# Kernel optimization log

Hardware: AMD Instinct MI355X
Metric: run time of the kernel (lower is better)

## Reference

```python
import jax, jax.numpy as jnp
import numpy as np

B = 4             # graphs per batch
POS_RANGE = 240.0 # pos lives in [0, 240)^3
VOXELS = (20.0, 30.0, 50.0, 80.0)
NEG = -1e30


def _basis(u):
    # open B-spline basis, degree 1, kernel_size 2, dim 3 -> 8 weights per edge
    cols = []
    for k in range(8):
        w = (u[:, 0] if k & 4 else 1.0 - u[:, 0])
        w = w * (u[:, 1] if k & 2 else 1.0 - u[:, 1])
        w = w * (u[:, 2] if k & 1 else 1.0 - u[:, 2])
        cols.append(w)
    return jnp.stack(cols, axis=1)  # [E, 8]


def _cartesian(pos, src, dst, emask):
    # T.Cartesian(cat=False, norm=True): rel pos scaled into [0,1]
    rel = pos[src] - pos[dst]
    m = jnp.max(jnp.where(emask[:, None], jnp.abs(rel), 0.0))
    return rel / (2.0 * jnp.maximum(m, 1e-9)) + 0.5


def _spline_conv(x, src, dst, pseudo, emask, W, Wr, b, n_nodes):
    # out_i = mean_{j->i} sum_k B_k(u_ij) x_j W_k + x_i Wr + b
    basis = _basis(pseudo) * emask[:, None].astype(x.dtype)  # [E,8]
    xk = jnp.einsum('ni,kio->nko', x, W)                     # [N,8,O]
    msg = basis[:, 0, None] * xk[src, 0]
    for k in range(1, 8):
        msg = msg + basis[:, k, None] * xk[src, k]           # [E,O]
    agg = jax.ops.segment_sum(msg, dst, num_segments=n_nodes)
    deg = jax.ops.segment_sum(emask.astype(x.dtype), dst, num_segments=n_nodes)
    return agg / jnp.maximum(deg, 1.0)[:, None] + x @ Wr + b


def _voxel_ids(pos, batch, vs):
    G = int(np.ceil(POS_RANGE / vs))
    c = jnp.clip(jnp.floor(pos / vs).astype(jnp.int64), 0, G - 1)
    cell = (c[:, 0] * G + c[:, 1]) * G + c[:, 2]
    return batch * (G ** 3) + cell, G ** 3


def _max_pool(x, pos, batch, valid, src, dst, emask, vs):
    # voxel-grid max pooling: nodes become fixed voxel cells (empty cells masked)
    nid, ncells = _voxel_ids(pos, batch, vs)
    n_new = B * ncells
    xm = jnp.where(valid[:, None], x, NEG)
    x_p = jax.ops.segment_max(xm, nid, num_segments=n_new)
    cnt = jax.ops.segment_sum(valid.astype(x.dtype), nid, num_segments=n_new)
    v_new = cnt > 0
    x_p = jnp.where(v_new[:, None], x_p, 0.0)
    pos_p = jax.ops.segment_sum(pos * valid[:, None].astype(pos.dtype), nid, num_segments=n_new)
    pos_p = pos_p / jnp.maximum(cnt, 1.0)[:, None]
    batch_p = jnp.arange(n_new, dtype=jnp.int64) // ncells
    # coarsen edges: remap to cells, drop self loops, coalesce at fixed size
    s2, d2 = nid[src], nid[dst]
    sent = n_new * n_new
    key = jnp.where(emask & (s2 != d2), s2 * n_new + d2, sent)
    uk = jnp.unique(key, size=key.shape[0], fill_value=sent)
    em = uk != sent
    uk = jnp.where(em, uk, 0)
    return x_p, pos_p, batch_p, v_new, uk // n_new, uk % n_new, em


def setup_inputs():
    key = jax.random.key(0)
    ks = jax.random.split(key, 24)
    NP, DEG = 5000, 8
    N = B * NP
    E = N * DEG
    x = jax.random.normal(ks[0], (N, 1), dtype=jnp.float32)
    pos = jax.random.uniform(ks[1], (N, 3), dtype=jnp.float32) * POS_RANGE
    src = jnp.repeat(jnp.arange(N, dtype=jnp.int64), DEG)
    delta = jax.random.randint(ks[2], (E,), 1, 100, dtype=jnp.int64)
    dst = (src // NP) * NP + (src % NP + delta) % NP   # intra-graph edges
    edge_index = jnp.stack([src, dst])
    batch = jnp.arange(N, dtype=jnp.int64) // NP
    sizes = [1, 64, 128, 256, 512]
    params = {}
    for l in range(4):
        ci, co = sizes[l], sizes[l + 1]
        params[f'W{l+1}'] = jax.random.normal(ks[3 + 3 * l], (8, ci, co), dtype=jnp.float32) / np.sqrt(8.0 * ci)
        params[f'Wr{l+1}'] = jax.random.normal(ks[4 + 3 * l], (ci, co), dtype=jnp.float32) / np.sqrt(float(ci))
        params[f'b{l+1}'] = jnp.zeros((co,), dtype=jnp.float32)
    params['fc1_w'] = jax.random.normal(ks[16], (64 * 512, 1024), dtype=jnp.float32) / np.sqrt(64.0 * 512.0)
    params['fc1_b'] = jnp.zeros((1024,), dtype=jnp.float32)
    params['fc2_w'] = jax.random.normal(ks[17], (1024, 1), dtype=jnp.float32) / np.sqrt(1024.0)
    params['fc2_b'] = jnp.zeros((1,), dtype=jnp.float32)
    return dict(x=x, pos=pos, edge_index=edge_index, batch=batch, **params)


def reference(x, pos, edge_index, batch, W1, Wr1, b1, W2, Wr2, b2, W3, Wr3, b3,
              W4, Wr4, b4, fc1_w, fc1_b, fc2_w, fc2_b):
    src, dst = edge_index[0], edge_index[1]
    n_nodes = x.shape[0]
    valid = jnp.ones((n_nodes,), dtype=bool)
    emask = jnp.ones((src.shape[0],), dtype=bool)
    Ws = [(W1, Wr1, b1), (W2, Wr2, b2), (W3, Wr3, b3), (W4, Wr4, b4)]
    for l in range(4):
        pseudo = _cartesian(pos, src, dst, emask)
        W, Wr, b = Ws[l]
        x = jax.nn.elu(_spline_conv(x, src, dst, pseudo, emask, W, Wr, b, n_nodes))
        if l < 3:
            x, pos, batch, valid, src, dst, emask = _max_pool(x, pos, batch, valid, src, dst, emask, VOXELS[l])
            n_nodes = x.shape[0]
    # MaxPoolingX(voxel=80, size=64): ceil(240/80)^3 = 27 <= 64 slots per graph
    nid, ncells = _voxel_ids(pos, batch, VOXELS[3])
    cluster = batch * 64 + (nid % ncells)
    xm = jnp.where(valid[:, None], x, NEG)
    xg = jax.ops.segment_max(xm, cluster, num_segments=B * 64)
    xg = jnp.where(xg <= NEG / 2, 0.0, xg)      # empty slots -> 0 (scatter-max default)
    xg = xg.reshape(B, 64 * 512)
    h = jax.nn.elu(xg @ fc1_w + fc1_b)           # dropout = identity (eval mode)
    return jax.nn.elu(h @ fc2_w + fc2_b)         # [B, 1]
```

## Files before the change

kernel.cpp:

```cpp
#include <hip/hip_runtime.h>

static constexpr int E0 = 160000;
static constexpr int NL0 = 20000;
static constexpr int NL1 = 6912;
static constexpr int NL2 = 2048;
static constexpr int NL3 = 500;

typedef short bf16x8 __attribute__((ext_vector_type(8)));
typedef float f32x4 __attribute__((ext_vector_type(4)));

__device__ __forceinline__ unsigned f2ord(float f) {
  unsigned u = __float_as_uint(f);
  return (u & 0x80000000u) ? ~u : (u | 0x80000000u);
}
__device__ __forceinline__ float ord2f(unsigned u) {
  unsigned v = (u & 0x80000000u) ? (u & 0x7fffffffu) : ~u;
  return __uint_as_float(v);
}
__device__ __forceinline__ float eluf(float x) { return x > 0.f ? x : expm1f(x); }
__device__ __forceinline__ void basis8(float u0, float u1, float u2, float* w) {
  float a0 = 1.f - u0, a1 = 1.f - u1, a2 = 1.f - u2;
  w[0] = a0*a1*a2; w[1] = a0*a1*u2; w[2] = a0*u1*a2; w[3] = a0*u1*u2;
  w[4] = u0*a1*a2; w[5] = u0*a1*u2; w[6] = u0*u1*a2; w[7] = u0*u1*u2;
}
__device__ __forceinline__ unsigned short f2b(float f) {
  unsigned u = __float_as_uint(f);
  return (unsigned short)((u + 0x7fffu + ((u >> 16) & 1u)) >> 16);
}
__device__ __forceinline__ float b2f(unsigned short h) {
  return __uint_as_float(((unsigned)h) << 16);
}
__device__ __forceinline__ int clampi(int v, int lo, int hi) {
  return v < lo ? lo : (v > hi ? hi : v);
}

__device__ __forceinline__ void mfma_tile(const unsigned short* __restrict__ Ah,
    const unsigned short* __restrict__ Al, const unsigned short* __restrict__ Bh,
    const unsigned short* __restrict__ Bl, int M, long K, int m0, int n0,
    int kbeg, int ksl, char* smem, f32x4* acc) {
  auto Ash = (unsigned short (*)[40])(smem);
  auto Asl = (unsigned short (*)[40])(smem + 5120);
  auto Bsh = (unsigned short (*)[40])(smem + 10240);
  auto Bsl = (unsigned short (*)[40])(smem + 15360);
  int t = threadIdx.x;
  int r = t >> 2, sg = (t & 3) * 8;
  int w = t >> 6, lane = t & 63;
  int ar = (w << 4) + (lane & 15), kq = (lane >> 4) << 3;
  for (int kt = 0; kt < ksl; kt += 32) {
    bf16x8 va = {}, vl = {};
    if (m0 + r < M) {
      long ga = (long)(m0 + r) * K + kbeg + kt + sg;
      va = *(const bf16x8*)&Ah[ga];
      vl = *(const bf16x8*)&Al[ga];
    }
    *(bf16x8*)&Ash[r][sg] = va;
    *(bf16x8*)&Asl[r][sg] = vl;
    long gb = (long)(n0 + r) * K + kbeg + kt + sg;
    *(bf16x8*)&Bsh[r][sg] = *(const bf16x8*)&Bh[gb];
    *(bf16x8*)&Bsl[r][sg] = *(const bf16x8*)&Bl[gb];
    __syncthreads();
    bf16x8 ah = *(const bf16x8*)&Ash[ar][kq];
    bf16x8 al = *(const bf16x8*)&Asl[ar][kq];
    #pragma unroll
    for (int nt = 0; nt < 4; nt++) {
      int br = (nt << 4) + (lane & 15);
      bf16x8 bh = *(const bf16x8*)&Bsh[br][kq];
      bf16x8 bl = *(const bf16x8*)&Bsl[br][kq];
      acc[nt] = __builtin_amdgcn_mfma_f32_16x16x32_bf16(al, bh, acc[nt], 0, 0, 0);
      acc[nt] = __builtin_amdgcn_mfma_f32_16x16x32_bf16(ah, bl, acc[nt], 0, 0, 0);
      acc[nt] = __builtin_amdgcn_mfma_f32_16x16x32_bf16(ah, bh, acc[nt], 0, 0, 0);
    }
    __syncthreads();
  }
}

__global__ __launch_bounds__(256)
void k_prep(const int* __restrict__ src0, const int* __restrict__ dst0,
            const float* __restrict__ pos0, int* __restrict__ head0,
            int* __restrict__ next0, float* __restrict__ mbuf,
            const float* __restrict__ W1, const float* __restrict__ Wr1, float* __restrict__ wc1,
            const float* __restrict__ W2, const float* __restrict__ Wr2,
            const float* __restrict__ W3, const float* __restrict__ Wr3,
            const float* __restrict__ W4, const float* __restrict__ Wr4,
            unsigned short* __restrict__ w2h, unsigned short* __restrict__ w2l,
            unsigned short* __restrict__ w3h, unsigned short* __restrict__ w3l,
            unsigned short* __restrict__ w4h, unsigned short* __restrict__ w4l) {
  __shared__ __align__(16) float T[64][65];
  __shared__ float red[4];
  int tid = blockIdx.x * 256 + threadIdx.x, gsz = gridDim.x * 256;
  float v = 0.f;
  for (int e = tid; e < E0; e += gsz) {
    int s = src0[e], d = dst0[e];
    next0[e] = atomicExch(&head0[d], e + 1);
    v = fmaxf(v, fabsf(pos0[s*3]   - pos0[d*3]));
    v = fmaxf(v, fabsf(pos0[s*3+1] - pos0[d*3+1]));
    v = fmaxf(v, fabsf(pos0[s*3+2] - pos0[d*3+2]));
  }
  #pragma unroll
  for (int off = 32; off; off >>= 1) v = fmaxf(v, __shfl_down(v, off, 64));
  if ((threadIdx.x & 63) == 0) red[threadIdx.x >> 6] = v;
  __syncthreads();
  if (threadIdx.x == 0)
    atomicMax((unsigned*)mbuf,
              __float_as_uint(fmaxf(fmaxf(red[0], red[1]), fmaxf(red[2], red[3]))));
  for (int b = blockIdx.x; b < 378; b += gridDim.x) {
    const float *W, *Wr; unsigned short *oh, *ol; int K, N, kt, nt;
    if (b < 18)      { W = W2; Wr = Wr2; oh = w2h; ol = w2l; K = 576;  N = 128; kt = b / 2; nt = b % 2; }
    else if (b < 90) { int q = b - 18; W = W3; Wr = Wr3; oh = w3h; ol = w3l; K = 1152; N = 256; kt = q / 4; nt = q % 4; }
    else             { int q = b - 90; W = W4; Wr = Wr4; oh = w4h; ol = w4l; K = 2304; N = 512; kt = q / 8; nt = q % 8; }
    int k0 = kt * 64, n0 = nt * 64, KW = K - K / 9;
    __syncthreads();
    for (int i = threadIdx.x; i < 4096; i += 256) {
      int kk = i >> 6, nn = i & 63, k = k0 + kk;
      T[kk][nn] = (k < KW) ? W[(long)k * N + n0 + nn] : Wr[(long)(k - KW) * N + n0 + nn];
    }
    __syncthreads();
    for (int i = threadIdx.x; i < 4096; i += 256) {
      int nn = i >> 6, kk = i & 63;
      float vv = T[kk][nn];
      unsigned short hu = f2b(vv), lu = f2b(vv - b2f(hu));
      long o = (long)(n0 + nn) * K + k0 + kk;
      oh[o] = hu; ol[o] = lu;
    }
  }
  if (blockIdx.x == 0)
    for (int i = threadIdx.x; i < 576; i += 256)
      wc1[i] = (i < 512) ? W1[i] : Wr1[i - 512];
}

__global__ __launch_bounds__(256)
void k_l1(const float* __restrict__ pos0, const float* __restrict__ x0,
          const int* __restrict__ src0, const int* __restrict__ head0,
          const int* __restrict__ next0, const float* __restrict__ mbuf,
          const float* __restrict__ wc1, const float* __restrict__ b1,
          unsigned* __restrict__ pord1, float* __restrict__ cnt1,
          float* __restrict__ possum1, int* __restrict__ nid) {
  int d = blockIdx.x * 4 + (threadIdx.x >> 6);
  int lane = threadIdx.x & 63;
  if (d >= NL0) return;
  float inv = 0.5f / fmaxf(mbuf[0], 1e-9f);
  float pd0 = pos0[d*3], pd1 = pos0[d*3+1], pd2 = pos0[d*3+2];
  float acc[8] = {};
  int len = 0;
  for (int j = head0[d]; j; ) {
    int e = j - 1; j = next0[e];
    int s = src0[e];
    float u0 = (pos0[s*3]   - pd0) * inv + 0.5f;
    float u1 = (pos0[s*3+1] - pd1) * inv + 0.5f;
    float u2 = (pos0[s*3+2] - pd2) * inv + 0.5f;
    float w[8]; basis8(u0, u1, u2, w);
    float xv = x0[s];
    #pragma unroll
    for (int k = 0; k < 8; k++) acc[k] += w[k] * xv;
    len++;
  }
  float sc = 1.f / fmaxf((float)len, 1.f);
  float v = b1[lane] + x0[d] * wc1[512 + lane];
  #pragma unroll
  for (int k = 0; k < 8; k++) v += acc[k] * sc * wc1[k * 64 + lane];
  v = eluf(v);
  int c0 = clampi((int)floorf(pd0 / 20.f), 0, 11);
  int c1 = clampi((int)floorf(pd1 / 20.f), 0, 11);
  int c2 = clampi((int)floorf(pd2 / 20.f), 0, 11);
  int id = (d / 5000) * 1728 + (c0 * 12 + c1) * 12 + c2;
  atomicMax(&pord1[(long)id * 64 + lane], f2ord(v));
  if (lane == 0) {
    nid[d] = id;
    atomicAdd(&cnt1[id], 1.f);
    atomicAdd(&possum1[id*3],   pd0);
    atomicAdd(&possum1[id*3+1], pd1);
    atomicAdd(&possum1[id*3+2], pd2);
  }
}

__global__ __launch_bounds__(256)
void k_pedge(const int* __restrict__ srcf, const int* __restrict__ dstf,
             const int* __restrict__ ecntf, int ecap,
             const int* __restrict__ nid, int Nn, unsigned* __restrict__ bitmap,
             int* __restrict__ srcc, int* __restrict__ dstc, int* __restrict__ nextc,
             int* __restrict__ headc, int* __restrict__ ecntc,
             const float* __restrict__ possum, const float* __restrict__ cnt,
             float* __restrict__ mo) {
  __shared__ float red[4];
  int n = ecntf ? *ecntf : ecap;
  float vmax = 0.f;
  for (int e = blockIdx.x * 256 + threadIdx.x; e < n; e += gridDim.x * 256) {
    int s2 = nid[srcf[e]], d2 = nid[dstf[e]];
    if (s2 == d2) continue;
    float ics = 1.f / fmaxf(cnt[s2], 1.f), icd = 1.f / fmaxf(cnt[d2], 1.f);
    vmax = fmaxf(vmax, fabsf(possum[s2*3]   * ics - possum[d2*3]   * icd));
    vmax = fmaxf(vmax, fabsf(possum[s2*3+1] * ics - possum[d2*3+1] * icd));
    vmax = fmaxf(vmax, fabsf(possum[s2*3+2] * ics - possum[d2*3+2] * icd));
    unsigned key = (unsigned)s2 * (unsigned)Nn + (unsigned)d2;
    unsigned bit = 1u << (key & 31);
    unsigned old = atomicOr(&bitmap[key >> 5], bit);
    if (!(old & bit)) {
      int q = atomicAdd(ecntc, 1);
      srcc[q] = s2; dstc[q] = d2;
      nextc[q] = atomicExch(&headc[d2], q + 1);
    }
  }
  #pragma unroll
  for (int off = 32; off; off >>= 1) vmax = fmaxf(vmax, __shfl_down(vmax, off, 64));
  if ((threadIdx.x & 63) == 0) red[threadIdx.x >> 6] = vmax;
  __syncthreads();
  if (threadIdx.x == 0)
    atomicMax((unsigned*)mo,
              __float_as_uint(fmaxf(fmaxf(red[0], red[1]), fmaxf(red[2], red[3]))));
}

__global__ __launch_bounds__(256)
void k_gather(const float* __restrict__ possum, const float* __restrict__ cnt,
              const unsigned* __restrict__ pordc,
              const int* __restrict__ srcarr, const int* __restrict__ head,
              const int* __restrict__ nextl, const float* __restrict__ mbuf,
              unsigned short* __restrict__ ysh, unsigned short* __restrict__ ysl,
              int N, int Ci, int nchunk) {
  int wid = blockIdx.x * 4 + (threadIdx.x >> 6);
  int lane = threadIdx.x & 63;
  int d = wid / nchunk, ch = wid % nchunk;
  if (d >= N) return;
  int co = ch * 64 + lane;
  float inv = 0.5f / fmaxf(mbuf[0], 1e-9f);
  float cd = cnt[d];
  float icd = 1.f / fmaxf(cd, 1.f);
  float pd0 = possum[d*3] * icd, pd1 = possum[d*3+1] * icd, pd2 = possum[d*3+2] * icd;
  float acc[8] = {};
  int len = 0;
  for (int j = head[d]; j; ) {
    int e = j - 1; j = nextl[e];
    int s = srcarr[e];
    float ics = 1.f / fmaxf(cnt[s], 1.f);
    float u0 = (possum[s*3]   * ics - pd0) * inv + 0.5f;
    float u1 = (possum[s*3+1] * ics - pd1) * inv + 0.5f;
    float u2 = (possum[s*3+2] * ics - pd2) * inv + 0.5f;
    float w[8]; basis8(u0, u1, u2, w);
    float xv = ord2f(pordc[(long)s * Ci + co]);
    #pragma unroll
    for (int k = 0; k < 8; k++) acc[k] += w[k] * xv;
    len++;
  }
  float sc = 1.f / fmaxf((float)len, 1.f);
  long row = (long)d * 9 * Ci;
  #pragma unroll
  for (int k = 0; k < 8; k++) {
    float v = acc[k] * sc;
    unsigned short hu = f2b(v);
    ysh[row + k * Ci + co] = hu;
    ysl[row + k * Ci + co] = f2b(v - b2f(hu));
  }
  float xd = (cd > 0.f) ? ord2f(pordc[(long)d * Ci + co]) : 0.f;
  unsigned short hu = f2b(xd);
  ysh[row + 8 * Ci + co] = hu;
  ysl[row + 8 * Ci + co] = f2b(xd - b2f(hu));
}

__global__ __launch_bounds__(256)
void k_gemmpool(const unsigned short* __restrict__ ysh, const unsigned short* __restrict__ ysl,
                const unsigned short* __restrict__ Bh, const unsigned short* __restrict__ Bl,
                int M, int N, int K, const float* __restrict__ bias,
                const float* __restrict__ possum, const float* __restrict__ cnt,
                int div, float vs, int G, int NC,
                unsigned* __restrict__ pordn, float* __restrict__ cntn,
                float* __restrict__ possumn, int* __restrict__ nid) {
  __shared__ __align__(16) char smem[20480];
  int nbx = N >> 6;
  int bx = blockIdx.x % nbx, by = blockIdx.x / nbx;
  int m0 = by * 64, n0 = bx * 64;
  f32x4 acc[4] = {};
  mfma_tile(ysh, ysl, Bh, Bl, M, K, m0, n0, 0, K, smem, acc);
  int w = threadIdx.x >> 6, lane = threadIdx.x & 63;
  int row0 = m0 + (w << 4) + ((lane >> 4) << 2);
  int colb = n0 + (lane & 15);
  #pragma unroll
  for (int q = 0; q < 4; q++) {
    int gm = row0 + q;
    float c = cnt[gm];
    float ic = 1.f / fmaxf(c, 1.f);
    float p0 = possum[gm*3] * ic, p1 = possum[gm*3+1] * ic, p2 = possum[gm*3+2] * ic;
    int c0 = clampi((int)floorf(p0 / vs), 0, G - 1);
    int c1 = clampi((int)floorf(p1 / vs), 0, G - 1);
    int c2 = clampi((int)floorf(p2 / vs), 0, G - 1);
    int id = (gm / div) * NC + (c0 * G + c1) * G + c2;
    bool vl = c > 0.f;
    if (bx == 0 && (lane & 15) == 0) {
      nid[gm] = id;
      if (vl) {
        atomicAdd(&cntn[id], 1.f);
        atomicAdd(&possumn[id*3],   p0);
        atomicAdd(&possumn[id*3+1], p1);
        atomicAdd(&possumn[id*3+2], p2);
      }
    }
    if (vl) {
      #pragma unroll
      for (int nt = 0; nt < 4; nt++) {
        int col = colb + nt * 16;
        float v = eluf(acc[nt][q] + bias[col]);
        atomicMax(&pordn[(long)id * N + col], f2ord(v));
      }
    }
  }
}

__global__ __launch_bounds__(256)
void k_gemm4(const unsigned short* __restrict__ ysh, const unsigned short* __restrict__ ysl,
             const unsigned short* __restrict__ Bh, const unsigned short* __restrict__ Bl,
             float* __restrict__ Cp) {
  __shared__ __align__(16) char smem[20480];
  int z = blockIdx.x >> 6, rem = blockIdx.x & 63, bx = rem & 7, by = rem >> 3;
  int m0 = by * 64, n0 = bx * 64;
  f32x4 acc[4] = {};
  mfma_tile(ysh, ysl, Bh, Bl, 500, 2304, m0, n0, z * 576, 576, smem, acc);
  float* Co = Cp + (long)z * 256000;
  int w = threadIdx.x >> 6, lane = threadIdx.x & 63;
  int row0 = m0 + (w << 4) + ((lane >> 4) << 2);
  int colb = n0 + (lane & 15);
  #pragma unroll
  for (int nt = 0; nt < 4; nt++)
    #pragma unroll
    for (int q = 0; q < 4; q++) {
      int gm = row0 + q;
      if (gm < 500) Co[(long)gm * 512 + colb + nt * 16] = acc[nt][q];
    }
}

__global__ void k_reduce4(const float* __restrict__ Cp, const float* __restrict__ b4,
                          const float* __restrict__ possum3, const float* __restrict__ cnt3,
                          unsigned* __restrict__ xg) {
  int idx = blockIdx.x * 256 + threadIdx.x;
  if (idx >= 256000) return;
  int n = idx >> 9, o = idx & 511;
  float s = Cp[idx] + Cp[idx + 256000] + Cp[idx + 512000] + Cp[idx + 768000];
  float v = eluf(s + b4[o]);
  float c = cnt3[n];
  if (c <= 0.f) return;
  float ic = 1.f / c;
  float p0 = possum3[n*3] * ic, p1 = possum3[n*3+1] * ic, p2 = possum3[n*3+2] * ic;
  int c0 = clampi((int)floorf(p0 / 80.f), 0, 2);
  int c1 = clampi((int)floorf(p1 / 80.f), 0, 2);
  int c2 = clampi((int)floorf(p2 / 80.f), 0, 2);
  int cl = (n / 125) * 64 + (c0 * 3 + c1) * 3 + c2;
  atomicMax(&xg[(long)cl * 512 + o], f2ord(v));
}

__global__ __launch_bounds__(128)
void k_fc1(const unsigned* __restrict__ xg_ord, const float* __restrict__ w,
           float* __restrict__ h) {
  int cellhalf = blockIdx.x >> 3, jb = blockIdx.x & 7;
  int cell = cellhalf >> 1, half = cellhalf & 1;
  int j = jb * 128 + threadIdx.x;
  __shared__ float xs[4][256];
  for (int q = threadIdx.x; q < 1024; q += 128) {
    int b = q >> 8, ci = q & 255;
    unsigned o = xg_ord[((b * 64 + cell) << 9) + half * 256 + ci];
    xs[b][ci] = (o == 0u) ? 0.f : ord2f(o);
  }
  __syncthreads();
  float a0 = 0, a1 = 0, a2 = 0, a3 = 0;
  int cbase = cell * 512 + half * 256;
  for (int ci = 0; ci < 256; ci++) {
    float ww = w[(long)(cbase + ci) * 1024 + j];
    a0 += xs[0][ci] * ww; a1 += xs[1][ci] * ww;
    a2 += xs[2][ci] * ww; a3 += xs[3][ci] * ww;
  }
  atomicAdd(&h[j], a0);        atomicAdd(&h[1024 + j], a1);
  atomicAdd(&h[2048 + j], a2); atomicAdd(&h[3072 + j], a3);
}

__global__ void k_fc2(const float* __restrict__ h, const float* __restrict__ fb1,
                      const float* __restrict__ w, const float* __restrict__ b,
                      float* __restrict__ out) {
  int bb = blockIdx.x, t = threadIdx.x;
  float a = 0;
  for (int j = t; j < 1024; j += 256) a += eluf(h[bb * 1024 + j] + fb1[j]) * w[j];
  for (int off = 32; off; off >>= 1) a += __shfl_down(a, off, 64);
  __shared__ float red[4];
  int lane = t & 63, wv = t >> 6;
  if (lane == 0) red[wv] = a;
  __syncthreads();
  if (t == 0) out[bb] = eluf(red[0] + red[1] + red[2] + red[3] + b[0]);
}

extern "C" void kernel_launch(void* const* d_in, const int* in_sizes, int n_in,
                              void* d_out, int out_size, void* d_ws, size_t ws_size,
                              hipStream_t stream) {
  const float* x0   = (const float*)d_in[0];
  const float* pos0 = (const float*)d_in[1];
  const int*   ei   = (const int*)d_in[2];
  const float* W1 = (const float*)d_in[4],  *Wr1 = (const float*)d_in[5],  *b1 = (const float*)d_in[6];
  const float* W2 = (const float*)d_in[7],  *Wr2 = (const float*)d_in[8],  *b2 = (const float*)d_in[9];
  const float* W3 = (const float*)d_in[10], *Wr3 = (const float*)d_in[11], *b3 = (const float*)d_in[12];
  const float* W4 = (const float*)d_in[13], *Wr4 = (const float*)d_in[14], *b4 = (const float*)d_in[15];
  const float* fw1 = (const float*)d_in[16], *fb1 = (const float*)d_in[17];
  const float* fw2 = (const float*)d_in[18], *fb2 = (const float*)d_in[19];
  float* out = (float*)d_out;
  const int* src0 = ei;
  const int* dst0 = ei + E0;

  char* ws = (char*)d_ws;
  size_t off = 0;
  auto alloc = [&](size_t bytes) -> void* {
    off = (off + 255) & ~(size_t)255;
    void* q = ws + off; off += bytes; return q;
  };
  int* next0 = (int*)alloc(E0 * 4);
  int* src1 = (int*)alloc(E0 * 4); int* dst1 = (int*)alloc(E0 * 4); int* next1 = (int*)alloc(E0 * 4);
  int* src2 = (int*)alloc(E0 * 4); int* dst2 = (int*)alloc(E0 * 4); int* next2 = (int*)alloc(E0 * 4);
  int* src3 = (int*)alloc(E0 * 4); int* dst3 = (int*)alloc(E0 * 4); int* next3 = (int*)alloc(E0 * 4);
  int* nid  = (int*)alloc(NL0 * 4);
  unsigned short* ysh = (unsigned short*)alloc((size_t)NL1 * 576 * 2);
  unsigned short* ysl = (unsigned short*)alloc((size_t)NL1 * 576 * 2);
  float* wc1 = (float*)alloc(576 * 4);
  unsigned short* w2h = (unsigned short*)alloc((size_t)576 * 128 * 2);
  unsigned short* w2l = (unsigned short*)alloc((size_t)576 * 128 * 2);
  unsigned short* w3h = (unsigned short*)alloc((size_t)1152 * 256 * 2);
  unsigned short* w3l = (unsigned short*)alloc((size_t)1152 * 256 * 2);
  unsigned short* w4h = (unsigned short*)alloc((size_t)2304 * 512 * 2);
  unsigned short* w4l = (unsigned short*)alloc((size_t)2304 * 512 * 2);
  float* Cp = (float*)alloc((size_t)4 * 256000 * 4);
  char* z0 = (char*)alloc(0);
  int* head0 = (int*)alloc(NL0 * 4);
  int* head1 = (int*)alloc(NL1 * 4);
  int* head2 = (int*)alloc(NL2 * 4);
  int* head3 = (int*)alloc(NL3 * 4);
  unsigned* pord1 = (unsigned*)alloc((size_t)NL1 * 64 * 4);
  unsigned* pord2 = (unsigned*)alloc((size_t)NL2 * 128 * 4);
  unsigned* pord3 = (unsigned*)alloc((size_t)NL3 * 256 * 4);
  unsigned* xg    = (unsigned*)alloc((size_t)4 * 64 * 512 * 4);
  float* cnt1 = (float*)alloc(NL1 * 4);
  float* cnt2 = (float*)alloc(NL2 * 4);
  float* cnt3 = (float*)alloc(NL3 * 4);
  float* possum1 = (float*)alloc(NL1 * 12);
  float* possum2 = (float*)alloc(NL2 * 12);
  float* possum3 = (float*)alloc(NL3 * 12);
  size_t bm1w = ((size_t)NL1 * NL1 + 31) / 32;
  size_t bm2w = ((size_t)NL2 * NL2 + 31) / 32;
  size_t bm3w = ((size_t)NL3 * NL3 + 31) / 32;
  unsigned* bm1 = (unsigned*)alloc(bm1w * 4);
  unsigned* bm2 = (unsigned*)alloc(bm2w * 4);
  unsigned* bm3 = (unsigned*)alloc(bm3w * 4);
  float* mbuf = (float*)alloc(64);
  int* ecnt = (int*)(mbuf + 8);
  float* h = (float*)alloc(4096 * 4);
  char* zend = (char*)alloc(0);
  size_t zbytes = (size_t)(zend - z0);
  (void)ws_size; (void)in_sizes; (void)n_in; (void)out_size;

  auto cdiv = [](long a, long b) { return (int)((a + b - 1) / b); };

  hipMemsetAsync(z0, 0, zbytes, stream);

  k_prep<<<512, 256, 0, stream>>>(src0, dst0, pos0, head0, next0, mbuf,
                                  W1, Wr1, wc1, W2, Wr2, W3, Wr3, W4, Wr4,
                                  w2h, w2l, w3h, w3l, w4h, w4l);
  k_l1<<<cdiv(NL0, 4), 256, 0, stream>>>(pos0, x0, src0, head0, next0, mbuf,
                                         wc1, b1, pord1, cnt1, possum1, nid);
  k_pedge<<<512, 256, 0, stream>>>(src0, dst0, nullptr, E0, nid, NL1, bm1,
                                   src1, dst1, next1, head1, ecnt + 0,
                                   possum1, cnt1, mbuf + 1);
  k_gather<<<cdiv(NL1, 4), 256, 0, stream>>>(possum1, cnt1, pord1, src1, head1, next1,
                                             mbuf + 1, ysh, ysl, NL1, 64, 1);
  k_gemmpool<<<(128 / 64) * (NL1 / 64), 256, 0, stream>>>(
      ysh, ysl, w2h, w2l, NL1, 128, 576, b2, possum1, cnt1,
      1728, 30.f, 8, 512, pord2, cnt2, possum2, nid);
  k_pedge<<<512, 256, 0, stream>>>(src1, dst1, ecnt + 0, E0, nid, NL2, bm2,
                                   src2, dst2, next2, head2, ecnt + 1,
                                   possum2, cnt2, mbuf + 2);
  k_gather<<<cdiv(NL2 * 2, 4), 256, 0, stream>>>(possum2, cnt2, pord2, src2, head2, next2,
                                                 mbuf + 2, ysh, ysl, NL2, 128, 2);
  k_gemmpool<<<(256 / 64) * (NL2 / 64), 256, 0, stream>>>(
      ysh, ysl, w3h, w3l, NL2, 256, 1152, b3, possum2, cnt2,
      512, 50.f, 5, 125, pord3, cnt3, possum3, nid);
  k_pedge<<<512, 256, 0, stream>>>(src2, dst2, ecnt + 1, E0, nid, NL3, bm3,
                                   src3, dst3, next3, head3, ecnt + 2,
                                   possum3, cnt3, mbuf + 3);
  k_gather<<<cdiv(NL3 * 4, 4), 256, 0, stream>>>(possum3, cnt3, pord3, src3, head3, next3,
                                                 mbuf + 3, ysh, ysl, NL3, 256, 4);
  k_gemm4<<<256, 256, 0, stream>>>(ysh, ysl, w4h, w4l, Cp);
  k_reduce4<<<cdiv(256000, 256), 256, 0, stream>>>(Cp, b4, possum3, cnt3, xg);
  k_fc1<<<27 * 2 * 8, 128, 0, stream>>>(xg, fw1, h);
  k_fc2<<<4, 256, 0, stream>>>(h, fb1, fw2, fb2, out);
}
```

Before: 427.6 us.

## Replace linked-list adjacency with CSR edge records carrying precomputed relative positions

The per-destination linked lists built with atomicExch are replaced by a degree count, an atomic row allocation and a scatter pass. This produces contiguous per-destination edge records (source id or x, plus relative position). Gathers now stream int4 records instead of chasing next pointers and re-deriving cluster positions. Layer 1 is also reorganised so that one thread handles one node's edge loop and the 64-wide output is computed from shared memory. The gather loop is unrolled by two. The cost is two extra kernel launches per layer and an extra scatter pass with atomics.

```diff
diff --git a/kernel.cpp b/kernel.cpp
--- a/kernel.cpp
+++ b/kernel.cpp
@@ -76,8 +76,8 @@
 
 __global__ __launch_bounds__(256)
 void k_prep(const int* __restrict__ src0, const int* __restrict__ dst0,
-            const float* __restrict__ pos0, int* __restrict__ head0,
-            int* __restrict__ next0, float* __restrict__ mbuf,
+            const float* __restrict__ pos0, const float* __restrict__ x0,
+            int* __restrict__ degi, int4* __restrict__ erec0u, float* __restrict__ mbuf,
             const float* __restrict__ W1, const float* __restrict__ Wr1, float* __restrict__ wc1,
             const float* __restrict__ W2, const float* __restrict__ Wr2,
             const float* __restrict__ W3, const float* __restrict__ Wr3,
@@ -91,10 +91,13 @@
   float v = 0.f;
   for (int e = tid; e < E0; e += gsz) {
     int s = src0[e], d = dst0[e];
-    next0[e] = atomicExch(&head0[d], e + 1);
-    v = fmaxf(v, fabsf(pos0[s*3]   - pos0[d*3]));
-    v = fmaxf(v, fabsf(pos0[s*3+1] - pos0[d*3+1]));
-    v = fmaxf(v, fabsf(pos0[s*3+2] - pos0[d*3+2]));
+    atomicAdd(&degi[d], 1);
+    float r0 = pos0[s*3]   - pos0[d*3];
+    float r1 = pos0[s*3+1] - pos0[d*3+1];
+    float r2 = pos0[s*3+2] - pos0[d*3+2];
+    erec0u[e] = make_int4(__float_as_int(x0[s]), __float_as_int(r0),
+                          __float_as_int(r1), __float_as_int(r2));
+    v = fmaxf(v, fmaxf(fabsf(r0), fmaxf(fabsf(r1), fabsf(r2))));
   }
   #pragma unroll
   for (int off = 32; off; off >>= 1) v = fmaxf(v, __shfl_down(v, off, 64));
@@ -128,76 +131,118 @@
       wc1[i] = (i < 512) ? W1[i] : Wr1[i - 512];
 }
 
+__global__ void k_alloc(int* __restrict__ degi, int* __restrict__ rowbeg,
+                        int* __restrict__ rowlen, int* __restrict__ cursor,
+                        int* __restrict__ ctr, int N) {
+  int n = blockIdx.x * 256 + threadIdx.x;
+  if (n >= N) return;
+  int len = degi[n];
+  int st = atomicAdd(ctr, len);
+  rowbeg[n] = st; cursor[n] = st; rowlen[n] = len; degi[n] = 0;
+}
+
+__global__ void k_scat(const int4* __restrict__ eu, const int* __restrict__ du,
+                       const int* __restrict__ ecnt, int ecap,
+                       int* __restrict__ cursor, int4* __restrict__ es) {
+  int n = ecnt ? *ecnt : ecap;
+  for (int e = blockIdx.x * 256 + threadIdx.x; e < n; e += gridDim.x * 256) {
+    int p = atomicAdd(&cursor[du[e]], 1);
+    es[p] = eu[e];
+  }
+}
+
 __global__ __launch_bounds__(256)
 void k_l1(const float* __restrict__ pos0, const float* __restrict__ x0,
-          const int* __restrict__ src0, const int* __restrict__ head0,
-          const int* __restrict__ next0, const float* __restrict__ mbuf,
+          const int4* __restrict__ erec, const int* __restrict__ rowbeg,
+          const int* __restrict__ rowlen, const float* __restrict__ mbuf,
           const float* __restrict__ wc1, const float* __restrict__ b1,
           unsigned* __restrict__ pord1, float* __restrict__ cnt1,
           float* __restrict__ possum1, int* __restrict__ nid) {
-  int d = blockIdx.x * 4 + (threadIdx.x >> 6);
-  int lane = threadIdx.x & 63;
-  if (d >= NL0) return;
+  __shared__ float ys9[256][12];
+  int t = threadIdx.x;
+  int d = blockIdx.x * 256 + t;
   float inv = 0.5f / fmaxf(mbuf[0], 1e-9f);
-  float pd0 = pos0[d*3], pd1 = pos0[d*3+1], pd2 = pos0[d*3+2];
-  float acc[8] = {};
-  int len = 0;
-  for (int j = head0[d]; j; ) {
-    int e = j - 1; j = next0[e];
-    int s = src0[e];
-    float u0 = (pos0[s*3]   - pd0) * inv + 0.5f;
-    float u1 = (pos0[s*3+1] - pd1) * inv + 0.5f;
-    float u2 = (pos0[s*3+2] - pd2) * inv + 0.5f;
-    float w[8]; basis8(u0, u1, u2, w);
-    float xv = x0[s];
+  if (d < NL0) {
+    int beg = rowbeg[d], len = rowlen[d];
+    float acc[8] = {};
+    for (int j = beg; j < beg + len; j++) {
+      int4 rc = erec[j];
+      float xv = __int_as_float(rc.x);
+      float u0 = __int_as_float(rc.y) * inv + 0.5f;
+      float u1 = __int_as_float(rc.z) * inv + 0.5f;
+      float u2 = __int_as_float(rc.w) * inv + 0.5f;
+      float w[8]; basis8(u0, u1, u2, w);
+      #pragma unroll
+      for (int k = 0; k < 8; k++) acc[k] += w[k] * xv;
+    }
+    float sc = 1.f / fmaxf((float)len, 1.f);
     #pragma unroll
-    for (int k = 0; k < 8; k++) acc[k] += w[k] * xv;
-    len++;
-  }
-  float sc = 1.f / fmaxf((float)len, 1.f);
-  float v = b1[lane] + x0[d] * wc1[512 + lane];
+    for (int k = 0; k < 8; k++) ys9[t][k] = acc[k] * sc;
+    ys9[t][8]  = x0[d];
+    ys9[t][9]  = pos0[d*3];
+    ys9[t][10] = pos0[d*3+1];
+    ys9[t][11] = pos0[d*3+2];
+  }
+  __syncthreads();
+  int lane = t & 63, wv = t >> 6;
+  float wcol[9];
   #pragma unroll
-  for (int k = 0; k < 8; k++) v += acc[k] * sc * wc1[k * 64 + lane];
-  v = eluf(v);
-  int c0 = clampi((int)floorf(pd0 / 20.f), 0, 11);
-  int c1 = clampi((int)floorf(pd1 / 20.f), 0, 11);
-  int c2 = clampi((int)floorf(pd2 / 20.f), 0, 11);
-  int id = (d / 5000) * 1728 + (c0 * 12 + c1) * 12 + c2;
-  atomicMax(&pord1[(long)id * 64 + lane], f2ord(v));
-  if (lane == 0) {
-    nid[d] = id;
-    atomicAdd(&cnt1[id], 1.f);
-    atomicAdd(&possum1[id*3],   pd0);
-    atomicAdd(&possum1[id*3+1], pd1);
-    atomicAdd(&possum1[id*3+2], pd2);
+  for (int k = 0; k < 8; k++) wcol[k] = wc1[k * 64 + lane];
+  wcol[8] = wc1[512 + lane];
+  float bb = b1[lane];
+  int base = blockIdx.x * 256 + wv * 64;
+  for (int i = 0; i < 64; i++) {
+    int dd = base + i;
+    if (dd >= NL0) break;
+    int li = wv * 64 + i;
+    float v = bb + ys9[li][8] * wcol[8];
+    #pragma unroll
+    for (int k = 0; k < 8; k++) v += ys9[li][k] * wcol[k];
+    v = eluf(v);
+    float pd0 = ys9[li][9], pd1 = ys9[li][10], pd2 = ys9[li][11];
+    int c0 = clampi((int)floorf(pd0 / 20.f), 0, 11);
+    int c1 = clampi((int)floorf(pd1 / 20.f), 0, 11);
+    int c2 = clampi((int)floorf(pd2 / 20.f), 0, 11);
+    int id = (dd / 5000) * 1728 + (c0 * 12 + c1) * 12 + c2;
+    atomicMax(&pord1[(long)id * 64 + lane], f2ord(v));
+    if (lane == 0) {
+      nid[dd] = id;
+      atomicAdd(&cnt1[id], 1.f);
+      atomicAdd(&possum1[id*3],   pd0);
+      atomicAdd(&possum1[id*3+1], pd1);
+      atomicAdd(&possum1[id*3+2], pd2);
+    }
   }
 }
 
 __global__ __launch_bounds__(256)
-void k_pedge(const int* __restrict__ srcf, const int* __restrict__ dstf,
-             const int* __restrict__ ecntf, int ecap,
+void k_pedge(const int4* __restrict__ erecf, const int* __restrict__ srcf,
+             const int* __restrict__ dstf, const int* __restrict__ ecntf, int ecap,
              const int* __restrict__ nid, int Nn, unsigned* __restrict__ bitmap,
-             int* __restrict__ srcc, int* __restrict__ dstc, int* __restrict__ nextc,
-             int* __restrict__ headc, int* __restrict__ ecntc,
-             const float* __restrict__ possum, const float* __restrict__ cnt,
-             float* __restrict__ mo) {
+             int4* __restrict__ erecu, int* __restrict__ dstu, int* __restrict__ ecntc,
+             int* __restrict__ degi, const float* __restrict__ possum,
+             const float* __restrict__ cnt, float* __restrict__ mo) {
   __shared__ float red[4];
   int n = ecntf ? *ecntf : ecap;
   float vmax = 0.f;
   for (int e = blockIdx.x * 256 + threadIdx.x; e < n; e += gridDim.x * 256) {
-    int s2 = nid[srcf[e]], d2 = nid[dstf[e]];
+    int sL = erecf ? erecf[e].x : srcf[e];
+    int dL = dstf[e];
+    int s2 = nid[sL], d2 = nid[dL];
     if (s2 == d2) continue;
     float ics = 1.f / fmaxf(cnt[s2], 1.f), icd = 1.f / fmaxf(cnt[d2], 1.f);
-    vmax = fmaxf(vmax, fabsf(possum[s2*3]   * ics - possum[d2*3]   * icd));
-    vmax = fmaxf(vmax, fabsf(possum[s2*3+1] * ics - possum[d2*3+1] * icd));
-    vmax = fmaxf(vmax, fabsf(possum[s2*3+2] * ics - possum[d2*3+2] * icd));
+    float r0 = possum[s2*3]   * ics - possum[d2*3]   * icd;
+    float r1 = possum[s2*3+1] * ics - possum[d2*3+1] * icd;
+    float r2 = possum[s2*3+2] * ics - possum[d2*3+2] * icd;
+    vmax = fmaxf(vmax, fmaxf(fabsf(r0), fmaxf(fabsf(r1), fabsf(r2))));
     unsigned key = (unsigned)s2 * (unsigned)Nn + (unsigned)d2;
     unsigned bit = 1u << (key & 31);
     unsigned old = atomicOr(&bitmap[key >> 5], bit);
     if (!(old & bit)) {
       int q = atomicAdd(ecntc, 1);
-      srcc[q] = s2; dstc[q] = d2;
-      nextc[q] = atomicExch(&headc[d2], q + 1);
+      erecu[q] = make_int4(s2, __float_as_int(r0), __float_as_int(r1), __float_as_int(r2));
+      dstu[q] = d2;
+      atomicAdd(&degi[d2], 1);
     }
   }
   #pragma unroll
@@ -210,10 +255,9 @@
 }
 
 __global__ __launch_bounds__(256)
-void k_gather(const float* __restrict__ possum, const float* __restrict__ cnt,
-              const unsigned* __restrict__ pordc,
-              const int* __restrict__ srcarr, const int* __restrict__ head,
-              const int* __restrict__ nextl, const float* __restrict__ mbuf,
+void k_gather(const unsigned* __restrict__ pordc, const int4* __restrict__ erec,
+              const int* __restrict__ rowbeg, const int* __restrict__ rowlen,
+              const float* __restrict__ mbuf,
               unsigned short* __restrict__ ysh, unsigned short* __restrict__ ysl,
               int N, int Ci, int nchunk) {
   int wid = blockIdx.x * 4 + (threadIdx.x >> 6);
@@ -222,23 +266,35 @@
   if (d >= N) return;
   int co = ch * 64 + lane;
   float inv = 0.5f / fmaxf(mbuf[0], 1e-9f);
-  float cd = cnt[d];
-  float icd = 1.f / fmaxf(cd, 1.f);
-  float pd0 = possum[d*3] * icd, pd1 = possum[d*3+1] * icd, pd2 = possum[d*3+2] * icd;
+  int beg = rowbeg[d], len = rowlen[d], end = beg + len;
   float acc[8] = {};
-  int len = 0;
-  for (int j = head[d]; j; ) {
-    int e = j - 1; j = nextl[e];
-    int s = srcarr[e];
-    float ics = 1.f / fmaxf(cnt[s], 1.f);
-    float u0 = (possum[s*3]   * ics - pd0) * inv + 0.5f;
-    float u1 = (possum[s*3+1] * ics - pd1) * inv + 0.5f;
-    float u2 = (possum[s*3+2] * ics - pd2) * inv + 0.5f;
-    float w[8]; basis8(u0, u1, u2, w);
-    float xv = ord2f(pordc[(long)s * Ci + co]);
+  int j = beg;
+  for (; j + 1 < end; j += 2) {
+    int4 ra = erec[j], rb = erec[j + 1];
+    float ua0 = __int_as_float(ra.y) * inv + 0.5f;
+    float ua1 = __int_as_float(ra.z) * inv + 0.5f;
+    float ua2 = __int_as_float(ra.w) * inv + 0.5f;
+    float ub0 = __int_as_float(rb.y) * inv + 0.5f;
+    float ub1 = __int_as_float(rb.z) * inv + 0.5f;
+    float ub2 = __int_as_float(rb.w) * inv + 0.5f;
+    float xa = ord2f(pordc[(long)ra.x * Ci + co]);
+    float xb = ord2f(pordc[(long)rb.x * Ci + co]);
+    float wa[8], wb[8];
+    basis8(ua0, ua1, ua2, wa);
+    basis8(ub0, ub1, ub2, wb);
     #pragma unroll
-    for (int k = 0; k < 8; k++) acc[k] += w[k] * xv;
-    len++;
+    for (int k = 0; k < 8; k++) acc[k] += wa[k] * xa + wb[k] * xb;
+  }
+  if (j < end) {
+    int4 ra = erec[j];
+    float ua0 = __int_as_float(ra.y) * inv + 0.5f;
+    float ua1 = __int_as_float(ra.z) * inv + 0.5f;
+    float ua2 = __int_as_float(ra.w) * inv + 0.5f;
+    float xa = ord2f(pordc[(long)ra.x * Ci + co]);
+    float wa[8];
+    basis8(ua0, ua1, ua2, wa);
+    #pragma unroll
+    for (int k = 0; k < 8; k++) acc[k] += wa[k] * xa;
   }
   float sc = 1.f / fmaxf((float)len, 1.f);
   long row = (long)d * 9 * Ci;
@@ -249,7 +305,9 @@
     ysh[row + k * Ci + co] = hu;
     ysl[row + k * Ci + co] = f2b(v - b2f(hu));
   }
-  float xd = (cd > 0.f) ? ord2f(pordc[(long)d * Ci + co]) : 0.f;
+  float xd = ord2f(pordc[(long)d * Ci + co]);
+  unsigned od = pordc[(long)d * Ci + co];
+  xd = (od == 0u) ? 0.f : ord2f(od);
   unsigned short hu = f2b(xd);
   ysh[row + 8 * Ci + co] = hu;
   ysl[row + 8 * Ci + co] = f2b(xd - b2f(hu));
@@ -404,11 +462,16 @@
     off = (off + 255) & ~(size_t)255;
     void* q = ws + off; off += bytes; return q;
   };
-  int* next0 = (int*)alloc(E0 * 4);
-  int* src1 = (int*)alloc(E0 * 4); int* dst1 = (int*)alloc(E0 * 4); int* next1 = (int*)alloc(E0 * 4);
-  int* src2 = (int*)alloc(E0 * 4); int* dst2 = (int*)alloc(E0 * 4); int* next2 = (int*)alloc(E0 * 4);
-  int* src3 = (int*)alloc(E0 * 4); int* dst3 = (int*)alloc(E0 * 4); int* next3 = (int*)alloc(E0 * 4);
+  int4* erec0u = (int4*)alloc((size_t)E0 * 16);
+  int4* erec_s = (int4*)alloc((size_t)E0 * 16);
+  int4* eu_a   = (int4*)alloc((size_t)E0 * 16);
+  int4* eu_b   = (int4*)alloc((size_t)E0 * 16);
+  int* du_a = (int*)alloc(E0 * 4);
+  int* du_b = (int*)alloc(E0 * 4);
   int* nid  = (int*)alloc(NL0 * 4);
+  int* rowbeg = (int*)alloc(NL0 * 4);
+  int* rowlen = (int*)alloc(NL0 * 4);
+  int* cursor = (int*)alloc(NL0 * 4);
   unsigned short* ysh = (unsigned short*)alloc((size_t)NL1 * 576 * 2);
   unsigned short* ysl = (unsigned short*)alloc((size_t)NL1 * 576 * 2);
   float* wc1 = (float*)alloc(576 * 4);
@@ -420,10 +483,6 @@
   unsigned short* w4l = (unsigned short*)alloc((size_t)2304 * 512 * 2);
   float* Cp = (float*)alloc((size_t)4 * 256000 * 4);
   char* z0 = (char*)alloc(0);
-  int* head0 = (int*)alloc(NL0 * 4);
-  int* head1 = (int*)alloc(NL1 * 4);
-  int* head2 = (int*)alloc(NL2 * 4);
-  int* head3 = (int*)alloc(NL3 * 4);
   unsigned* pord1 = (unsigned*)alloc((size_t)NL1 * 64 * 4);
   unsigned* pord2 = (unsigned*)alloc((size_t)NL2 * 128 * 4);
   unsigned* pord3 = (unsigned*)alloc((size_t)NL3 * 256 * 4);
@@ -440,8 +499,10 @@
   unsigned* bm1 = (unsigned*)alloc(bm1w * 4);
   unsigned* bm2 = (unsigned*)alloc(bm2w * 4);
   unsigned* bm3 = (unsigned*)alloc(bm3w * 4);
+  int* degi = (int*)alloc(NL0 * 4);
   float* mbuf = (float*)alloc(64);
   int* ecnt = (int*)(mbuf + 8);
+  int* ctr  = (int*)(mbuf + 12);
   float* h = (float*)alloc(4096 * 4);
   char* zend = (char*)alloc(0);
   size_t zbytes = (size_t)(zend - z0);
@@ -451,32 +512,37 @@
 
   hipMemsetAsync(z0, 0, zbytes, stream);
 
-  k_prep<<<512, 256, 0, stream>>>(src0, dst0, pos0, head0, next0, mbuf,
+  k_prep<<<512, 256, 0, stream>>>(src0, dst0, pos0, x0, degi, erec0u, mbuf,
                                   W1, Wr1, wc1, W2, Wr2, W3, Wr3, W4, Wr4,
                                   w2h, w2l, w3h, w3l, w4h, w4l);
-  k_l1<<<cdiv(NL0, 4), 256, 0, stream>>>(pos0, x0, src0, head0, next0, mbuf,
-                                         wc1, b1, pord1, cnt1, possum1, nid);
-  k_pedge<<<512, 256, 0, stream>>>(src0, dst0, nullptr, E0, nid, NL1, bm1,
-                                   src1, dst1, next1, head1, ecnt + 0,
-                                   possum1, cnt1, mbuf + 1);
-  k_gather<<<cdiv(NL1, 4), 256, 0, stream>>>(possum1, cnt1, pord1, src1, head1, next1,
-                                             mbuf + 1, ysh, ysl, NL1, 64, 1);
+  k_alloc<<<cdiv(NL0, 256), 256, 0, stream>>>(degi, rowbeg, rowlen, cursor, ctr + 0, NL0);
+  k_scat<<<512, 256, 0, stream>>>(erec0u, dst0, nullptr, E0, cursor, erec_s);
+  k_l1<<<cdiv(NL0, 256), 256, 0, stream>>>(pos0, x0, erec_s, rowbeg, rowlen, mbuf,
+                                           wc1, b1, pord1, cnt1, possum1, nid);
+  k_pedge<<<512, 256, 0, stream>>>(nullptr, src0, dst0, nullptr, E0, nid, NL1, bm1,
+                                   eu_a, du_a, ecnt + 0, degi, possum1, cnt1, mbuf + 1);
+  k_alloc<<<cdiv(NL1, 256), 256, 0, stream>>>(degi, rowbeg, rowlen, cursor, ctr + 1, NL1);
+  k_scat<<<512, 256, 0, stream>>>(eu_a, du_a, ecnt + 0, E0, cursor, erec_s);
+  k_gather<<<cdiv(NL1, 4), 256, 0, stream>>>(pord1, erec_s, rowbeg, rowlen, mbuf + 1,
+                                             ysh, ysl, NL1, 64, 1);
   k_gemmpool<<<(128 / 64) * (NL1 / 64), 256, 0, stream>>>(
       ysh, ysl, w2h, w2l, NL1, 128, 576, b2, possum1, cnt1,
       1728, 30.f, 8, 512, pord2, cnt2, possum2, nid);
-  k_pedge<<<512, 256, 0, stream>>>(src1, dst1, ecnt + 0, E0, nid, NL2, bm2,
-                                   src2, dst2, next2, head2, ecnt + 1,
-                                   possum2, cnt2, mbuf + 2);
-  k_gather<<<cdiv(NL2 * 2, 4), 256, 0, stream>>>(possum2, cnt2, pord2, src2, head2, next2,
-                                                 mbuf + 2, ysh, ysl, NL2, 128, 2);
+  k_pedge<<<512, 256, 0, stream>>>(eu_a, nullptr, du_a, ecnt + 0, E0, nid, NL2, bm2,
+                                   eu_b, du_b, ecnt + 1, degi, possum2, cnt2, mbuf + 2);
+  k_alloc<<<cdiv(NL2, 256), 256, 0, stream>>>(degi, rowbeg, rowlen, cursor, ctr + 2, NL2);
+  k_scat<<<512, 256, 0, stream>>>(eu_b, du_b, ecnt + 1, E0, cursor, erec_s);
+  k_gather<<<cdiv(NL2 * 2, 4), 256, 0, stream>>>(pord2, erec_s, rowbeg, rowlen, mbuf + 2,
+                                                 ysh, ysl, NL2, 128, 2);
   k_gemmpool<<<(256 / 64) * (NL2 / 64), 256, 0, stream>>>(
       ysh, ysl, w3h, w3l, NL2, 256, 1152, b3, possum2, cnt2,
       512, 50.f, 5, 125, pord3, cnt3, possum3, nid);
-  k_pedge<<<512, 256, 0, stream>>>(src2, dst2, ecnt + 1, E0, nid, NL3, bm3,
-                                   src3, dst3, next3, head3, ecnt + 2,
-                                   possum3, cnt3, mbuf + 3);
-  k_gather<<<cdiv(NL3 * 4, 4), 256, 0, stream>>>(possum3, cnt3, pord3, src3, head3, next3,
-                                                 mbuf + 3, ysh, ysl, NL3, 256, 4);
+  k_pedge<<<512, 256, 0, stream>>>(eu_b, nullptr, du_b, ecnt + 1, E0, nid, NL3, bm3,
+                                   eu_a, du_a, ecnt + 2, degi, possum3, cnt3, mbuf + 3);
+  k_alloc<<<cdiv(NL3, 256), 256, 0, stream>>>(degi, rowbeg, rowlen, cursor, ctr + 3, NL3);
+  k_scat<<<512, 256, 0, stream>>>(eu_a, du_a, ecnt + 2, E0, cursor, erec_s);
+  k_gather<<<cdiv(NL3 * 4, 4), 256, 0, stream>>>(pord3, erec_s, rowbeg, rowlen, mbuf + 3,
+                                                 ysh, ysl, NL3, 256, 4);
   k_gemm4<<<256, 256, 0, stream>>>(ysh, ysl, w4h, w4l, Cp);
   k_reduce4<<<cdiv(256000, 256), 256, 0, stream>>>(Cp, b4, possum3, cnt3, xg);
   k_fc1<<<27 * 2 * 8, 128, 0, stream>>>(xg, fw1, h);
```

After: 439.2 us. 2.7% more time.
